# Optimization experiments

Measured on AMD Instinct MI355X. Metric: run time of the kernel, lower is better.

Reference implementation:

```python
import jax, jax.numpy as jnp
import numpy as np

EMBED_DIM = 1024
NUM_HEADS = 16
HEAD_DIM = EMBED_DIM // NUM_HEADS
SCALE = HEAD_DIM ** -0.5


def setup_inputs() -> dict:
    key = jax.random.key(0)
    ks = jax.random.split(key, 9)
    B, S, D = 32, 577, EMBED_DIM
    std = 1.0 / np.sqrt(D)
    inp = {
        "hidden_states": jax.random.normal(ks[0], (B, S, D), dtype=jnp.float32),
        "q_w": jax.random.normal(ks[1], (D, D), dtype=jnp.float32) * std,
        "q_b": jax.random.normal(ks[2], (D,), dtype=jnp.float32) * 0.01,
        "k_w": jax.random.normal(ks[3], (D, D), dtype=jnp.float32) * std,
        "k_b": jax.random.normal(ks[4], (D,), dtype=jnp.float32) * 0.01,
        "v_w": jax.random.normal(ks[5], (D, D), dtype=jnp.float32) * std,
        "v_b": jax.random.normal(ks[6], (D,), dtype=jnp.float32) * 0.01,
        "o_w": jax.random.normal(ks[7], (D, D), dtype=jnp.float32) * std,
        "o_b": jax.random.normal(ks[8], (D,), dtype=jnp.float32) * 0.01,
    }
    return inp


def reference(hidden_states, q_w, q_b, k_w, k_b, v_w, v_b, o_w, o_b):
    B, S, D = hidden_states.shape
    H, Dh = NUM_HEADS, HEAD_DIM

    def proj(w, b):
        # torch Linear: x @ w.T + b ; reshape to [B, H, S, Dh]
        y = jnp.einsum('bsd,ed->bse', hidden_states, w) + b
        return y.reshape(B, S, H, Dh).transpose(0, 2, 1, 3)

    q = proj(q_w, q_b)
    k = proj(k_w, k_b)
    v = proj(v_w, v_b)

    scores = jnp.einsum('bhqd,bhkd->bhqk', q * SCALE, k)  # [B,H,S,S]
    attn = jax.nn.softmax(scores, axis=-1)
    out = jnp.einsum('bhqk,bhkd->bhqd', attn, v)  # [B,H,S,Dh]
    out = out.transpose(0, 2, 1, 3).reshape(B, S, D)
    return jnp.einsum('bsd,ed->bse', out, o_w) + o_b
```

## Files before the change

kernel.cpp:

```cpp
#include <hip/hip_runtime.h>
#include <hip/hip_bf16.h>
#include <stdint.h>

#define B_   32
#define S_   577
#define SP   640
#define D_   1024
#define H_   16
#define DH   64
#define BH_  (B_*H_)
#define M_   (B_*S_)
#define MP2  18688
#define SCALE_ 0.125f

typedef __bf16 bf16;
typedef __bf16 bf16x8 __attribute__((ext_vector_type(8)));
typedef __bf16 bf16x4 __attribute__((ext_vector_type(4)));
typedef float  f32x4  __attribute__((ext_vector_type(4)));

__device__ __forceinline__ void gload16(const bf16* g, bf16* l) {
    __builtin_amdgcn_global_load_lds((__attribute__((address_space(1))) void*)g,
                                     (__attribute__((address_space(3))) void*)l, 16, 0, 0);
}

__global__ void cast_kernel(const float* __restrict__ in, bf16* __restrict__ out, int n4) {
    int i = blockIdx.x * blockDim.x + threadIdx.x;
    if (i >= n4) return;
    float4 v = ((const float4*)in)[i];
    bf16x4 o;
    o[0] = (bf16)v.x; o[1] = (bf16)v.y; o[2] = (bf16)v.z; o[3] = (bf16)v.w;
    ((bf16x4*)out)[i] = o;
}

__global__ void cast4_kernel(const float* __restrict__ w0, const float* __restrict__ w1,
                             const float* __restrict__ w2, const float* __restrict__ w3,
                             bf16* __restrict__ o0, bf16* __restrict__ o1,
                             bf16* __restrict__ o2, bf16* __restrict__ o3) {
    int i = blockIdx.x * blockDim.x + threadIdx.x;
    int seg = i >> 18, r = i & 262143;
    const float* in = (seg == 0) ? w0 : (seg == 1) ? w1 : (seg == 2) ? w2 : w3;
    bf16* out       = (seg == 0) ? o0 : (seg == 1) ? o1 : (seg == 2) ? o2 : o3;
    float4 v = ((const float4*)in)[r];
    bf16x4 o;
    o[0] = (bf16)v.x; o[1] = (bf16)v.y; o[2] = (bf16)v.z; o[3] = (bf16)v.w;
    ((bf16x4*)out)[r] = o;
}

__device__ __forceinline__ void stage256(const bf16* __restrict__ A, const bf16* __restrict__ B,
                                         int m0, int n0, int K, int kt, bf16* SMbuf) {
    const int tid = threadIdx.x;
    const int wave = tid >> 6;
    #pragma unroll
    for (int ld = 0; ld < 8; ++ld) {
        int li  = ld * 512 + tid;
        int row = (li >> 3) & 255;
        int ch  = (li & 7) ^ (row & 7);
        const bf16* g = ((ld < 4) ? (A + (size_t)(m0 + row) * K)
                                  : (B + (size_t)(n0 + row) * K)) + kt * 64 + ch * 8;
        bf16* l = SMbuf + (size_t)(ld * 512 + wave * 64) * 8;
        gload16(g, l);
    }
}

__device__ __forceinline__ void compute256(const bf16* SMbuf, f32x4 acc[8][4],
                                           int wm, int wn, int r16, int c4) {
    #pragma unroll
    for (int kk = 0; kk < 2; ++kk) {
        bf16x8 bq[4];
        #pragma unroll
        for (int j = 0; j < 4; ++j) {
            int row = wn * 64 + j * 16 + r16;
            int c   = (kk * 4 + c4) ^ (row & 7);
            bq[j] = *(const bf16x8*)(SMbuf + 16384 + row * 64 + c * 8);
        }
        #pragma unroll
        for (int i = 0; i < 8; ++i) {
            int row = wm * 128 + i * 16 + r16;
            int c   = (kk * 4 + c4) ^ (row & 7);
            bf16x8 a = *(const bf16x8*)(SMbuf + row * 64 + c * 8);
            #pragma unroll
            for (int j = 0; j < 4; ++j)
                acc[i][j] = __builtin_amdgcn_mfma_f32_16x16x32_bf16(a, bq[j], acc[i][j], 0, 0, 0);
        }
    }
}

__global__ __launch_bounds__(512, 2) void gemm_qkv(const bf16* __restrict__ A, const bf16* __restrict__ Bw,
                                                   const float* __restrict__ qb, const float* __restrict__ kb,
                                                   const float* __restrict__ vb,
                                                   bf16* __restrict__ qk, bf16* __restrict__ vT) {
    __shared__ __align__(16) bf16 SM[2 * 32768];
    const int bx = blockIdx.x;
    const int bm = bx / 12, bn = bx % 12;
    const int m0 = bm * 256, n0 = bn * 256;
    const int tid = threadIdx.x;
    const int lane = tid & 63, wave = tid >> 6;
    const int wm = wave >> 2, wn = wave & 3;
    const int r16 = lane & 15, c4 = lane >> 4;

    f32x4 acc[8][4];
    #pragma unroll
    for (int i = 0; i < 8; ++i)
        #pragma unroll
        for (int j = 0; j < 4; ++j)
            #pragma unroll
            for (int r = 0; r < 4; ++r) acc[i][j][r] = 0.0f;

    stage256(A, Bw, m0, n0, 1024, 0, SM);
    __syncthreads();
    for (int kt = 0; kt < 16; ++kt) {
        if (kt < 15) stage256(A, Bw, m0, n0, 1024, kt + 1, SM + ((kt + 1) & 1) * 32768);
        compute256(SM + (kt & 1) * 32768, acc, wm, wn, r16, c4);
        __syncthreads();
    }

    if (bn < 8) {
        const float* barr = (bn < 4) ? qb : kb;
        const float mul = (bn < 4) ? SCALE_ : 1.0f;
        #pragma unroll
        for (int j = 0; j < 4; ++j) {
            int n = n0 + wn * 64 + j * 16 + r16;
            float bias = barr[n & 1023];
            #pragma unroll
            for (int i = 0; i < 8; ++i) {
                #pragma unroll
                for (int r = 0; r < 4; ++r) {
                    int m = m0 + wm * 128 + i * 16 + c4 * 4 + r;
                    if (m < M_) qk[(size_t)m * 2048 + n] = (bf16)((acc[i][j][r] + bias) * mul);
                }
            }
        }
    } else {
        const int bnp = bn - 8;
        bf16* Ts = SM;
        #pragma unroll
        for (int mh = 0; mh < 2; ++mh) {
            if (wm == mh) {
                #pragma unroll
                for (int j = 0; j < 4; ++j) {
                    int nl = wn * 64 + j * 16 + r16;
                    float bias = vb[bnp * 256 + nl];
                    #pragma unroll
                    for (int i = 0; i < 8; ++i) {
                        #pragma unroll
                        for (int r = 0; r < 4; ++r) {
                            int tr = i * 16 + c4 * 4 + r;
                            Ts[tr * 259 + nl] = (bf16)(acc[i][j][r] + bias);
                        }
                    }
                }
            }
            __syncthreads();
            {
                int ml = tid & 127, nh = tid >> 7;
                int gm = m0 + mh * 128 + ml;
                if (gm < M_) {
                    unsigned bb = (unsigned)gm / 577u, s = (unsigned)gm - bb * 577u;
                    bf16* dst = vT + ((size_t)((bb * 16 + bnp * 4 + nh) * 64)) * SP + s;
                    const bf16* src = Ts + ml * 259 + nh * 64;
                    #pragma unroll 8
                    for (int j = 0; j < 64; ++j) dst[(size_t)j * SP] = src[j];
                }
            }
            __syncthreads();
        }
    }
}

__global__ __launch_bounds__(512, 2) void gemm_out(const bf16* __restrict__ A, const bf16* __restrict__ Bw,
                                                   const float* __restrict__ ob, float* __restrict__ out) {
    __shared__ __align__(16) bf16 SM[2 * 32768];
    const int bx = blockIdx.x;
    const int bm = bx >> 2, bn = bx & 3;
    const int m0 = bm * 256, n0 = bn * 256;
    const int tid = threadIdx.x;
    const int lane = tid & 63, wave = tid >> 6;
    const int wm = wave >> 2, wn = wave & 3;
    const int r16 = lane & 15, c4 = lane >> 4;

    f32x4 acc[8][4];
    #pragma unroll
    for (int i = 0; i < 8; ++i)
        #pragma unroll
        for (int j = 0; j < 4; ++j)
            #pragma unroll
            for (int r = 0; r < 4; ++r) acc[i][j][r] = 0.0f;

    stage256(A, Bw, m0, n0, 1024, 0, SM);
    __syncthreads();
    for (int kt = 0; kt < 16; ++kt) {
        if (kt < 15) stage256(A, Bw, m0, n0, 1024, kt + 1, SM + ((kt + 1) & 1) * 32768);
        compute256(SM + (kt & 1) * 32768, acc, wm, wn, r16, c4);
        __syncthreads();
    }

    #pragma unroll
    for (int j = 0; j < 4; ++j) {
        int n = n0 + wn * 64 + j * 16 + r16;
        float bias = ob[n];
        #pragma unroll
        for (int i = 0; i < 8; ++i) {
            #pragma unroll
            for (int r = 0; r < 4; ++r) {
                int m = m0 + wm * 128 + i * 16 + c4 * 4 + r;
                if (m < M_) out[(size_t)m * 1024 + n] = acc[i][j][r] + bias;
            }
        }
    }
}

__global__ __launch_bounds__(256) void attn_kernel(const bf16* __restrict__ qk,
                                                   const bf16* __restrict__ vT, bf16* __restrict__ obuf) {
    __shared__ __align__(16) char Pls[4 * 2 * 2048];
    const int orig = blockIdx.x;
    const int xcd = orig & 7;
    const int t   = orig >> 3;
    const int qt  = t % 5, bhg = t / 5;
    const int bh  = bhg * 8 + xcd;
    const int b   = bh >> 4, h = bh & 15;
    const int lane = threadIdx.x & 63, wave = threadIdx.x >> 6;
    const int r16 = lane & 15, c4 = lane >> 4;
    const int q0  = qt * 128 + wave * 32;
    const int swz = (r16 & 7) << 4;

    const bf16* qp = qk + (size_t)(b * 577) * 2048 + h * 64;
    const bf16* kp = qp + 1024;
    const bf16* vp = vT + (size_t)bh * 64 * SP;

    bf16x8 aq[2][2];
    #pragma unroll
    for (int qf = 0; qf < 2; ++qf)
        #pragma unroll
        for (int c = 0; c < 2; ++c)
            aq[qf][c] = *(const bf16x8*)(qp + (size_t)(q0 + qf * 16 + r16) * 2048 + c * 32 + c4 * 8);

    float mi[2] = {-3.0e38f, -3.0e38f};
    float li[2] = {0.0f, 0.0f};
    f32x4 accO[2][4];
    #pragma unroll
    for (int qf = 0; qf < 2; ++qf)
        #pragma unroll
        for (int nt = 0; nt < 4; ++nt)
            #pragma unroll
            for (int r = 0; r < 4; ++r) accO[qf][nt][r] = 0.0f;

    char* pbase = Pls + wave * 4096 + r16 * 128;

    for (int kt = 0; kt < 10; ++kt) {
        bf16x8 kf[4][2];
        #pragma unroll
        for (int nt = 0; nt < 4; ++nt)
            #pragma unroll
            for (int c = 0; c < 2; ++c)
                kf[nt][c] = *(const bf16x8*)(kp + (size_t)(kt * 64 + nt * 16 + r16) * 2048 + c * 32 + c4 * 8);

        #pragma unroll
        for (int qf = 0; qf < 2; ++qf) {
            f32x4 sc[4];
            #pragma unroll
            for (int nt = 0; nt < 4; ++nt) {
                #pragma unroll
                for (int r = 0; r < 4; ++r) sc[nt][r] = 0.0f;
                #pragma unroll
                for (int c = 0; c < 2; ++c)
                    sc[nt] = __builtin_amdgcn_mfma_f32_16x16x32_bf16(kf[nt][c], aq[qf][c], sc[nt], 0, 0, 0);
            }
            if (kt == 9) {
                #pragma unroll
                for (int nt = 0; nt < 4; ++nt)
                    #pragma unroll
                    for (int r = 0; r < 4; ++r)
                        if (kt * 64 + nt * 16 + c4 * 4 + r >= S_) sc[nt][r] = -3.0e38f;
            }
            float pmax = sc[0][0];
            #pragma unroll
            for (int nt = 0; nt < 4; ++nt)
                #pragma unroll
                for (int r = 0; r < 4; ++r) pmax = fmaxf(pmax, sc[nt][r]);
            pmax = fmaxf(pmax, __shfl_xor(pmax, 16));
            pmax = fmaxf(pmax, __shfl_xor(pmax, 32));

            const bool vrow = (q0 + qf * 16 + r16) < S_;
            int ok = (!vrow) || (pmax <= mi[qf] + 8.0f);
            if (!__all(ok)) {
                float mnew = fmaxf(mi[qf], pmax);
                float fsc  = __expf(mi[qf] - mnew);
                mi[qf] = mnew;
                li[qf] *= fsc;
                float fs0 = __shfl(fsc, c4 * 4 + 0);
                float fs1 = __shfl(fsc, c4 * 4 + 1);
                float fs2 = __shfl(fsc, c4 * 4 + 2);
                float fs3 = __shfl(fsc, c4 * 4 + 3);
                #pragma unroll
                for (int nt = 0; nt < 4; ++nt) {
                    accO[qf][nt][0] *= fs0; accO[qf][nt][1] *= fs1;
                    accO[qf][nt][2] *= fs2; accO[qf][nt][3] *= fs3;
                }
            }
            float p[4][4];
            float rs = 0.0f;
            #pragma unroll
            for (int nt = 0; nt < 4; ++nt)
                #pragma unroll
                for (int r = 0; r < 4; ++r) {
                    p[nt][r] = __expf(sc[nt][r] - mi[qf]);
                    rs += p[nt][r];
                }
            rs += __shfl_xor(rs, 16);
            rs += __shfl_xor(rs, 32);
            li[qf] += rs;
            #pragma unroll
            for (int nt = 0; nt < 4; ++nt) {
                bf16x4 pk;
                pk[0] = (bf16)p[nt][0]; pk[1] = (bf16)p[nt][1];
                pk[2] = (bf16)p[nt][2]; pk[3] = (bf16)p[nt][3];
                *(bf16x4*)(pbase + qf * 2048 + ((nt * 32 + c4 * 8) ^ swz)) = pk;
            }
        }

        bf16x8 vf[4][2];
        #pragma unroll
        for (int ntd = 0; ntd < 4; ++ntd)
            #pragma unroll
            for (int kk = 0; kk < 2; ++kk)
                vf[ntd][kk] = *(const bf16x8*)(vp + (size_t)(ntd * 16 + r16) * SP + kt * 64 + kk * 32 + c4 * 8);
        #pragma unroll
        for (int qf = 0; qf < 2; ++qf) {
            bf16x8 pf[2];
            #pragma unroll
            for (int kk = 0; kk < 2; ++kk)
                pf[kk] = *(const bf16x8*)(pbase + qf * 2048 + ((kk * 64 + c4 * 16) ^ swz));
            #pragma unroll
            for (int ntd = 0; ntd < 4; ++ntd)
                #pragma unroll
                for (int kk = 0; kk < 2; ++kk)
                    accO[qf][ntd] = __builtin_amdgcn_mfma_f32_16x16x32_bf16(pf[kk], vf[ntd][kk], accO[qf][ntd], 0, 0, 0);
        }
    }

    #pragma unroll
    for (int qf = 0; qf < 2; ++qf) {
        float inv = 1.0f / li[qf];
        float rl0 = __shfl(inv, c4 * 4 + 0);
        float rl1 = __shfl(inv, c4 * 4 + 1);
        float rl2 = __shfl(inv, c4 * 4 + 2);
        float rl3 = __shfl(inv, c4 * 4 + 3);
        #pragma unroll
        for (int ntd = 0; ntd < 4; ++ntd) {
            #pragma unroll
            for (int r = 0; r < 4; ++r) {
                int s = q0 + qf * 16 + c4 * 4 + r;
                if (s < S_) {
                    float rl = (r == 0) ? rl0 : (r == 1) ? rl1 : (r == 2) ? rl2 : rl3;
                    obuf[((size_t)(b * S_ + s)) * 1024 + h * 64 + ntd * 16 + r16] =
                        (bf16)(accO[qf][ntd][r] * rl);
                }
            }
        }
    }
}

extern "C" void kernel_launch(void* const* d_in, const int* in_sizes, int n_in,
                              void* d_out, int out_size, void* d_ws, size_t ws_size,
                              hipStream_t stream) {
    const float* hs = (const float*)d_in[0];
    const float* qw = (const float*)d_in[1];
    const float* qb = (const float*)d_in[2];
    const float* kw = (const float*)d_in[3];
    const float* kb = (const float*)d_in[4];
    const float* vw = (const float*)d_in[5];
    const float* vb = (const float*)d_in[6];
    const float* ow = (const float*)d_in[7];
    const float* ob = (const float*)d_in[8];

    char* ws = (char*)d_ws;
    size_t off = 0;
    auto alloc = [&](size_t bytes) { void* p = ws + off; off += (bytes + 255) & ~255UL; return p; };
    bf16* hsA  = (bf16*)alloc((size_t)MP2 * 1024 * 2);
    bf16* wqkv = (bf16*)alloc((size_t)3072 * 1024 * 2);
    bf16* wo   = (bf16*)alloc((size_t)1024 * 1024 * 2);
    bf16* qk   = (bf16*)alloc((size_t)MP2 * 2048 * 2);
    bf16* vT   = (bf16*)alloc((size_t)BH_ * 64 * SP * 2);

    hipMemsetAsync(vT, 0, (size_t)BH_ * 64 * SP * 2, stream);

    int n4h = M_ * 1024 / 4;
    cast_kernel<<<(n4h + 255) / 256, 256, 0, stream>>>(hs, hsA, n4h);
    cast4_kernel<<<4096, 256, 0, stream>>>(qw, kw, vw, ow,
                                           wqkv, wqkv + 1048576, wqkv + 2097152, wo);

    gemm_qkv<<<73 * 12, 512, 0, stream>>>(hsA, wqkv, qb, kb, vb, qk, vT);
    attn_kernel<<<2560, 256, 0, stream>>>(qk, vT, hsA);
    gemm_out<<<73 * 4, 512, 0, stream>>>(hsA, wo, ob, (float*)d_out);
}
```

Baseline: 451.3 us.

## Prefetch next K tile, fold log2e into Q scale, use exp2 and setprio

Loads the first K tile before the attention loop and fetches the next K tile while softmax runs on the current scores, so global load latency is hidden behind compute. The softmax scale now includes log2(e) in the Q projection epilogue, which lets the kernel call the hardware exp2 directly instead of __expf. s_setprio raises wave priority around the MFMA blocks to help interleave matrix work across waves. The trade-off is higher register pressure from holding scores for both query fragments at once plus the prefetched K fragments.

```diff
diff --git a/kernel.cpp b/kernel.cpp
--- a/kernel.cpp
+++ b/kernel.cpp
@@ -12,6 +12,7 @@
 #define M_   (B_*S_)
 #define MP2  18688
 #define SCALE_ 0.125f
+#define LOG2E_ 1.44269504088896f
 
 typedef __bf16 bf16;
 typedef __bf16 bf16x8 __attribute__((ext_vector_type(8)));
@@ -116,7 +117,7 @@
 
     if (bn < 8) {
         const float* barr = (bn < 4) ? qb : kb;
-        const float mul = (bn < 4) ? SCALE_ : 1.0f;
+        const float mul = (bn < 4) ? SCALE_ * LOG2E_ : 1.0f;
         #pragma unroll
         for (int j = 0; j < 4; ++j) {
             int n = n0 + wn * 64 + j * 16 + r16;
@@ -246,37 +247,48 @@
 
     char* pbase = Pls + wave * 4096 + r16 * 128;
 
+    bf16x8 kf[4][2];
+    #pragma unroll
+    for (int nt = 0; nt < 4; ++nt)
+        #pragma unroll
+        for (int c = 0; c < 2; ++c)
+            kf[nt][c] = *(const bf16x8*)(kp + (size_t)(nt * 16 + r16) * 2048 + c * 32 + c4 * 8);
+
     for (int kt = 0; kt < 10; ++kt) {
-        bf16x8 kf[4][2];
-        #pragma unroll
-        for (int nt = 0; nt < 4; ++nt)
-            #pragma unroll
-            for (int c = 0; c < 2; ++c)
-                kf[nt][c] = *(const bf16x8*)(kp + (size_t)(kt * 64 + nt * 16 + r16) * 2048 + c * 32 + c4 * 8);
+        f32x4 sc[2][4];
+        __builtin_amdgcn_s_setprio(1);
+        #pragma unroll
+        for (int qf = 0; qf < 2; ++qf)
+            #pragma unroll
+            for (int nt = 0; nt < 4; ++nt) {
+                f32x4 z = {0.0f, 0.0f, 0.0f, 0.0f};
+                z = __builtin_amdgcn_mfma_f32_16x16x32_bf16(kf[nt][0], aq[qf][0], z, 0, 0, 0);
+                sc[qf][nt] = __builtin_amdgcn_mfma_f32_16x16x32_bf16(kf[nt][1], aq[qf][1], z, 0, 0, 0);
+            }
+        __builtin_amdgcn_s_setprio(0);
+
+        if (kt < 9) {
+            #pragma unroll
+            for (int nt = 0; nt < 4; ++nt)
+                #pragma unroll
+                for (int c = 0; c < 2; ++c)
+                    kf[nt][c] = *(const bf16x8*)(kp + (size_t)((kt + 1) * 64 + nt * 16 + r16) * 2048 + c * 32 + c4 * 8);
+        }
 
         #pragma unroll
         for (int qf = 0; qf < 2; ++qf) {
-            f32x4 sc[4];
-            #pragma unroll
-            for (int nt = 0; nt < 4; ++nt) {
-                #pragma unroll
-                for (int r = 0; r < 4; ++r) sc[nt][r] = 0.0f;
-                #pragma unroll
-                for (int c = 0; c < 2; ++c)
-                    sc[nt] = __builtin_amdgcn_mfma_f32_16x16x32_bf16(kf[nt][c], aq[qf][c], sc[nt], 0, 0, 0);
-            }
             if (kt == 9) {
                 #pragma unroll
                 for (int nt = 0; nt < 4; ++nt)
                     #pragma unroll
                     for (int r = 0; r < 4; ++r)
-                        if (kt * 64 + nt * 16 + c4 * 4 + r >= S_) sc[nt][r] = -3.0e38f;
-            }
-            float pmax = sc[0][0];
+                        if (576 + nt * 16 + c4 * 4 + r >= S_) sc[qf][nt][r] = -3.0e38f;
+            }
+            float pmax = sc[qf][0][0];
             #pragma unroll
             for (int nt = 0; nt < 4; ++nt)
                 #pragma unroll
-                for (int r = 0; r < 4; ++r) pmax = fmaxf(pmax, sc[nt][r]);
+                for (int r = 0; r < 4; ++r) pmax = fmaxf(pmax, sc[qf][nt][r]);
             pmax = fmaxf(pmax, __shfl_xor(pmax, 16));
             pmax = fmaxf(pmax, __shfl_xor(pmax, 32));
 
@@ -284,7 +296,7 @@
             int ok = (!vrow) || (pmax <= mi[qf] + 8.0f);
             if (!__all(ok)) {
                 float mnew = fmaxf(mi[qf], pmax);
-                float fsc  = __expf(mi[qf] - mnew);
+                float fsc  = __builtin_amdgcn_exp2f(mi[qf] - mnew);
                 mi[qf] = mnew;
                 li[qf] *= fsc;
                 float fs0 = __shfl(fsc, c4 * 4 + 0);
@@ -303,7 +315,7 @@
             for (int nt = 0; nt < 4; ++nt)
                 #pragma unroll
                 for (int r = 0; r < 4; ++r) {
-                    p[nt][r] = __expf(sc[nt][r] - mi[qf]);
+                    p[nt][r] = __builtin_amdgcn_exp2f(sc[qf][nt][r] - mi[qf]);
                     rs += p[nt][r];
                 }
             rs += __shfl_xor(rs, 16);
@@ -330,11 +342,13 @@
             #pragma unroll
             for (int kk = 0; kk < 2; ++kk)
                 pf[kk] = *(const bf16x8*)(pbase + qf * 2048 + ((kk * 64 + c4 * 16) ^ swz));
+            __builtin_amdgcn_s_setprio(1);
             #pragma unroll
             for (int ntd = 0; ntd < 4; ++ntd)
                 #pragma unroll
                 for (int kk = 0; kk < 2; ++kk)
                     accO[qf][ntd] = __builtin_amdgcn_mfma_f32_16x16x32_bf16(pf[kk], vf[ntd][kk], accO[qf][ntd], 0, 0, 0);
+            __builtin_amdgcn_s_setprio(0);
         }
     }
 
```

Result: no change. 453.6 us (+0.5%).
